# Kernel tuning notes

Measured on AMD Instinct MI355X. Metric: run time of the kernel, lower is better.

The kernel has to match this reference:

```python
import jax, jax.numpy as jnp
import numpy as np

B, H0, W0, D0 = 2, 28, 28, 28
C, NH, SR, WS = 96, 6, 4, 7
N = H0 * W0 * D0
EPS = 1e-5


def _window_partition(x, ws, H, W, D):
    # x: [B, heads, N, c] -> [B*heads*nWindows, ws^3, c]
    Bn, h, Nn, c = x.shape
    x = x.reshape(Bn * h, H // ws, ws, W // ws, ws, D // ws, ws, c)
    x = x.transpose(0, 1, 3, 5, 2, 4, 6, 7)
    return x.reshape(-1, ws * ws * ws, c)


def _window_reverse(w, ws, H, W, D, heads):
    # w: [B*heads*nWindows, ws^3, c] -> [B, N, heads*c]
    c = w.shape[-1]
    nW = (H // ws) * (W // ws) * (D // ws)
    Bh = w.shape[0] // nW
    x = w.reshape(Bh, H // ws, W // ws, D // ws, ws, ws, ws, c)
    x = x.transpose(0, 1, 4, 2, 5, 3, 6, 7).reshape(Bh, H, W, D, c)
    x = x.reshape(Bh // heads, heads, H, W, D, c).transpose(0, 2, 3, 4, 1, 5)
    return x.reshape(Bh // heads, H * W * D, heads * c)


def _ln(x, g, b):
    mu = x.mean(-1, keepdims=True)
    var = ((x - mu) ** 2).mean(-1, keepdims=True)
    return (x - mu) * jax.lax.rsqrt(var + EPS) * g + b


def _forward(x, H, W, D, lepe_lin_w, lepe_lin_b, lepe_conv_w, lepe_conv_b,
             sr_w, sr_b, norm_g, norm_b, q1_w, kv1_w, q2_w, kv2_w, proj_w, proj_b):
    Bn, Nn, Cc = x.shape
    nh2 = NH // 2
    hd = Cc // NH
    scale = hd ** -0.5
    dn = ('NCDHW', 'OIDHW', 'NCDHW')
    # LePE branch: linear -> depthwise 3x3x3 conv over the 3D volume
    t = (x @ lepe_lin_w.T + lepe_lin_b).transpose(0, 2, 1).reshape(Bn, Cc, H, W, D)
    lepe = jax.lax.conv_general_dilated(t, lepe_conv_w, (1, 1, 1), [(1, 1)] * 3,
                                        dimension_numbers=dn, feature_group_count=Cc)
    lepe = (lepe + lepe_conv_b[None, :, None, None, None]).reshape(Bn, Cc, Nn).transpose(0, 2, 1)
    # Branch 1: spatial-reduction global attention on half the heads
    q1 = (x @ q1_w.T).reshape(Bn, Nn, nh2, hd).transpose(0, 2, 1, 3)  # [B,h/2,N,hd]
    x5 = x.transpose(0, 2, 1).reshape(Bn, Cc, H, W, D)
    xs = jax.lax.conv_general_dilated(x5, sr_w, (SR, SR, SR), 'VALID', dimension_numbers=dn)
    xs = (xs + sr_b[None, :, None, None, None]).reshape(Bn, Cc, -1).transpose(0, 2, 1)  # [B,Nsr,C]
    xs = jax.nn.gelu(_ln(xs, norm_g, norm_b), approximate=False)
    kv1 = (xs @ kv1_w.T).reshape(Bn, -1, 2, nh2, hd).transpose(2, 0, 3, 1, 4)
    k1, v1 = kv1[0], kv1[1]
    attn1 = jax.nn.softmax(jnp.einsum('bhnd,bhmd->bhnm', q1, k1) * scale, axis=-1)
    x1 = jnp.einsum('bhnm,bhmd->bhnd', attn1, v1).transpose(0, 2, 1, 3).reshape(Bn, Nn, Cc // 2)
    # Branch 2: 7x7x7 windowed local attention on the other half of the heads
    q2 = (x @ q2_w.T).reshape(Bn, Nn, nh2, hd).transpose(0, 2, 1, 3)
    kv2 = (x @ kv2_w.T).reshape(Bn, Nn, 2, nh2, hd).transpose(2, 0, 3, 1, 4)
    k2, v2 = kv2[0], kv2[1]
    q2w = _window_partition(q2, WS, H, W, D)
    k2w = _window_partition(k2, WS, H, W, D)
    v2w = _window_partition(v2, WS, H, W, D)
    attn2 = jax.nn.softmax(jnp.einsum('wnd,wmd->wnm', q2w, k2w) * scale, axis=-1)
    x2 = _window_reverse(jnp.einsum('wnm,wmd->wnd', attn2, v2w), WS, H, W, D, nh2)
    # Fuse branches, add LePE, project
    return (jnp.concatenate([x1, x2], axis=-1) + lepe) @ proj_w.T + proj_b


def setup_inputs() -> dict:
    key = jax.random.key(0)
    ks = jax.random.split(key, 10)
    lin = lambda k, o, i: jax.random.normal(k, (o, i), jnp.float32) * 0.02
    return {
        'x': jax.random.normal(ks[0], (B, N, C), jnp.float32),
        'H': H0, 'W': W0, 'D': D0,
        'lepe_lin_w': lin(ks[1], C, C),
        'lepe_lin_b': jnp.zeros((C,), jnp.float32),
        'lepe_conv_w': jax.random.normal(ks[2], (C, 1, 3, 3, 3), jnp.float32) * 0.27,
        'lepe_conv_b': jnp.zeros((C,), jnp.float32),
        'sr_w': jax.random.normal(ks[3], (C, C, SR, SR, SR), jnp.float32) * 0.02,
        'sr_b': jnp.zeros((C,), jnp.float32),
        'norm_g': jnp.ones((C,), jnp.float32),
        'norm_b': jnp.zeros((C,), jnp.float32),
        'q1_w': lin(ks[4], C // 2, C),
        'kv1_w': lin(ks[5], C, C),
        'q2_w': lin(ks[6], C // 2, C),
        'kv2_w': lin(ks[7], C, C),
        'proj_w': lin(ks[8], C, C),
        'proj_b': jnp.zeros((C,), jnp.float32),
    }


def reference(x, H, W, D, lepe_lin_w, lepe_lin_b, lepe_conv_w, lepe_conv_b,
              sr_w, sr_b, norm_g, norm_b, q1_w, kv1_w, q2_w, kv2_w, proj_w, proj_b):
    return _forward(x, H, W, D, lepe_lin_w, lepe_lin_b, lepe_conv_w, lepe_conv_b,
                    sr_w, sr_b, norm_g, norm_b, q1_w, kv1_w, q2_w, kv2_w, proj_w, proj_b)
```

## Files before the change

### kernel.cpp

```cpp
#include <hip/hip_runtime.h>

#define BB 2
#define NTOK 21952
#define CC 96
#define WD 784
#define NSR 343
#define NKT 22
#define NPADK 9.f
#define NSITE 686
#define SCALE 0.25f
#define LN_EPS 1e-5f
#define WSA_N (6*16*24*64)
#define WPA_N (18*6*64)
#define PSTR 192
#define PLANE ((size_t)BB * NTOK)

typedef _Float16 half_t;
typedef __attribute__((ext_vector_type(2))) _Float16 h2;
typedef __attribute__((ext_vector_type(4))) _Float16 h4;
typedef __attribute__((ext_vector_type(8))) _Float16 h8;
typedef __attribute__((ext_vector_type(4))) float f32x4;
union HU { h8 v; h2 p[4]; };
union H4U { h4 v; h2 p[2]; };

__device__ __forceinline__ h2 pk2(float a, float b) {
    return __builtin_bit_cast(h2, __builtin_amdgcn_cvt_pkrtz(a, b));
}

__global__ __launch_bounds__(256) void k_wt(
    const float* __restrict__ w, h4* __restrict__ WSA, h4* __restrict__ WPA,
    const float* __restrict__ lepe_w, const float* __restrict__ q1_w,
    const float* __restrict__ q2_w, const float* __restrict__ kv2_w,
    const float* __restrict__ cw, float* __restrict__ cwT)
{
    const int id = blockIdx.x * 256 + threadIdx.x;
    if (id < WSA_N) {
        const int lane = id & 63;
        const int kt = (id >> 6) % 24;
        const int ks = ((id >> 6) / 24) % 16;
        const int ct = (id >> 6) / 384;
        const int co = ct * 16 + (lane & 15);
        const int kb = ks * 384 + kt * 16 + 4 * (lane >> 4);
        const int p = kb / 96, c = kb % 96;
        float f[4];
#pragma unroll
        for (int i = 0; i < 4; i++)
            f[i] = w[(size_t)co * 6144 + (c + i) * 64 + p];
        H4U t; t.p[0] = pk2(f[0], f[1]); t.p[1] = pk2(f[2], f[3]);
        WSA[id] = t.v;
    } else if (id < WSA_N + WPA_N) {
        const int id2 = id - WSA_N;
        const int lane = id2 & 63;
        const int kt = (id2 >> 6) % 6;
        const int ct = (id2 >> 6) / 6;
        const int co = ct * 16 + (lane & 15);
        const int k = kt * 16 + 4 * (lane >> 4);
        const float* wrow;
        if (co < 96)       wrow = lepe_w + co * 96;
        else if (co < 144) wrow = q1_w + (co - 96) * 96;
        else if (co < 192) wrow = q2_w + (co - 144) * 96;
        else               wrow = kv2_w + (co - 192) * 96;
        float4 v = *(const float4*)(wrow + k);
        H4U t; t.p[0] = pk2(v.x, v.y); t.p[1] = pk2(v.z, v.w);
        WPA[id2] = t.v;
    } else if (id < WSA_N + WPA_N + 27 * 96) {
        const int id3 = id - WSA_N - WPA_N;
        const int tap = id3 / 96, c = id3 % 96;
        cwT[tap * 96 + c] = cw[c * 27 + tap];
    }
}

__global__ __launch_bounds__(256) void k_proj(
    const float* __restrict__ x, const h4* __restrict__ WPA,
    const float* __restrict__ lepe_b, float* __restrict__ P,
    float4* __restrict__ tl)
{
    __shared__ h4 BX[4 * 6 * 64];
    const int blk = blockIdx.x;
    const int tid = threadIdx.x;

    for (int s = tid; s < 1536; s += 256) {
        int lane = s & 63;
        int kt = (s >> 6) % 6;
        int tt = (s >> 6) / 6;
        int tok = blk * 64 + tt * 16 + (lane & 15);
        int k0 = kt * 16 + 4 * (lane >> 4);
        float4 v = *(const float4*)(x + (size_t)tok * 96 + k0);
        H4U t; t.p[0] = pk2(v.x, v.y); t.p[1] = pk2(v.z, v.w);
        BX[s] = t.v;
    }
    __syncthreads();

    const int lane = tid & 63;
    const int wid = tid >> 6;

    h4 bx[24];
#pragma unroll
    for (int q = 0; q < 24; q++) bx[q] = BX[q * 64 + lane];

    for (int ct = wid; ct < 18; ct += 4) {
        f32x4 acc[4];
#pragma unroll
        for (int tt = 0; tt < 4; tt++) acc[tt] = (f32x4){0.f, 0.f, 0.f, 0.f};
#pragma unroll
        for (int kt = 0; kt < 6; kt++) {
            h4 wa = WPA[(ct * 6 + kt) * 64 + lane];
#pragma unroll
            for (int tt = 0; tt < 4; tt++)
                acc[tt] = __builtin_amdgcn_mfma_f32_16x16x16f16(
                    wa, bx[tt * 6 + kt], acc[tt], 0, 0, 0);
        }
        if (ct < 6) {
            float4 b4 = *(const float4*)(lepe_b + ct * 16 + 4 * (lane >> 4));
            const size_t cg = ct * 4 + (lane >> 4);
#pragma unroll
            for (int tt = 0; tt < 4; tt++) {
                int tok = blk * 64 + tt * 16 + (lane & 15);
                tl[cg * PLANE + tok] =
                    make_float4(acc[tt][0] + b4.x, acc[tt][1] + b4.y,
                                acc[tt][2] + b4.z, acc[tt][3] + b4.w);
            }
        } else {
#pragma unroll
            for (int tt = 0; tt < 4; tt++) {
                int tok = blk * 64 + tt * 16 + (lane & 15);
                *(float4*)(P + (size_t)tok * PSTR + (ct - 6) * 16
                           + 4 * (lane >> 4)) =
                    make_float4(acc[tt][0], acc[tt][1], acc[tt][2], acc[tt][3]);
            }
        }
    }
}

__global__ __launch_bounds__(384) void k_sr_a(
    const float* __restrict__ x, const h4* __restrict__ WSA,
    float* __restrict__ pa)
{
    __shared__ h4 BX[24 * 64];
    const int mb = blockIdx.x;
    const int ks = blockIdx.y;
    const int tid = threadIdx.x;
    const int lane = tid & 63;
    const int ct = tid >> 6;

    for (int s = tid; s < 24 * 64; s += 384) {
        int l = s & 63;
        int kt = s >> 6;
        int site = mb * 16 + (l & 15);
        if (site > NSITE - 1) site = NSITE - 1;
        int b = site / NSR, sloc = site % NSR;
        int si = sloc / 49, sj = (sloc / 7) % 7, sk = sloc % 7;
        int kg = ks * 384 + kt * 16 + 4 * (l >> 4);
        int p = kg / 96, c = kg % 96;
        int a = p >> 4, q = (p >> 2) & 3, r = p & 3;
        int n = (4 * si + a) * WD + (4 * sj + q) * 28 + (4 * sk + r);
        float4 v = *(const float4*)(x + ((size_t)b * NTOK + n) * 96 + c);
        H4U t; t.p[0] = pk2(v.x, v.y); t.p[1] = pk2(v.z, v.w);
        BX[s] = t.v;
    }
    __syncthreads();

    const int site_g = mb * 16 + (lane & 15);
    const h4* wb = WSA + (size_t)((ct * 16 + ks) * 24) * 64 + lane;

    f32x4 acc0 = (f32x4){0.f, 0.f, 0.f, 0.f};
    f32x4 acc1 = (f32x4){0.f, 0.f, 0.f, 0.f};
#pragma unroll
    for (int kp = 0; kp < 12; kp++) {
        h4 wa0 = wb[(2 * kp) * 64];
        h4 wa1 = wb[(2 * kp + 1) * 64];
        acc0 = __builtin_amdgcn_mfma_f32_16x16x16f16(
            wa0, BX[(2 * kp) * 64 + lane], acc0, 0, 0, 0);
        acc1 = __builtin_amdgcn_mfma_f32_16x16x16f16(
            wa1, BX[(2 * kp + 1) * 64 + lane], acc1, 0, 0, 0);
    }
    if (site_g < NSITE) {
        *(float4*)(pa + ((size_t)site_g * 16 + ks) * 96 + ct * 16
                   + 4 * (lane >> 4)) =
            make_float4(acc0[0] + acc1[0], acc0[1] + acc1[1],
                        acc0[2] + acc1[2], acc0[3] + acc1[3]);
    }
}

__global__ __launch_bounds__(96) void k_sr_b(
    const float* __restrict__ pa, const float* __restrict__ sr_b,
    const float* __restrict__ norm_g, const float* __restrict__ norm_b,
    const float* __restrict__ kv1_w, float* __restrict__ k1,
    float* __restrict__ v1)
{
    __shared__ float xs_s[96];
    __shared__ float gx[96];
    const int s_g = blockIdx.x;
    const int b = s_g / NSR, s = s_g % NSR;
    const int co = threadIdx.x;

    const float* pp = pa + (size_t)s_g * 16 * 96 + co;
    float acc = sr_b[co];
#pragma unroll
    for (int ks = 0; ks < 16; ks++) acc += pp[ks * 96];
    xs_s[co] = acc;
    __syncthreads();

    float m = 0.f, m2 = 0.f;
    for (int c = 0; c < 96; c++) { float v = xs_s[c]; m += v; m2 += v * v; }
    m *= (1.f / 96.f);
    float var = m2 * (1.f / 96.f) - m * m;
    float t = (acc - m) * rsqrtf(var + LN_EPS) * norm_g[co] + norm_b[co];
    gx[co] = 0.5f * t * (1.f + erff(t * 0.70710678118654752f));
    __syncthreads();

    const float4* w4 = (const float4*)(kv1_w + co * 96);
    const float4* g4 = (const float4*)gx;
    float a2 = 0.f;
#pragma unroll
    for (int c = 0; c < 24; c++) {
        float4 w = w4[c]; float4 g = g4[c];
        a2 += g.x * w.x + g.y * w.y + g.z * w.z + g.w * w.w;
    }
    int pair = co / 48, h = (co % 48) / 16, e = co % 16;
    float* dst = pair ? v1 : k1;
    dst[(((size_t)b * 3 + h) * NSR + s) * 16 + e] = a2;
}

__device__ __forceinline__ void attn_mfma_core(
    const h4* __restrict__ KA, const h4* __restrict__ VA, int lane,
    h4 qb, f32x4& o, float& lsum)
{
    o = (f32x4){0.f, 0.f, 0.f, 0.f};
    lsum = 0.f;
    for (int t = 0; t < NKT; t++) {
        h4 ka = KA[t * 64 + lane];
        f32x4 s = __builtin_amdgcn_mfma_f32_16x16x16f16(
            ka, qb, (f32x4){0.f, 0.f, 0.f, 0.f}, 0, 0, 0);
        float p0 = __expf(s[0]), p1 = __expf(s[1]);
        float p2 = __expf(s[2]), p3 = __expf(s[3]);
        lsum += (p0 + p1) + (p2 + p3);
        H4U pb;
        pb.p[0] = pk2(p0, p1);
        pb.p[1] = pk2(p2, p3);
        h4 va = VA[t * 64 + lane];
        o = __builtin_amdgcn_mfma_f32_16x16x16f16(va, pb.v, o, 0, 0, 0);
    }
}

__global__ __launch_bounds__(512) void k_attn(
    const float* __restrict__ P, const float* __restrict__ k1,
    const float* __restrict__ v1, float4* __restrict__ yp)
{
    __shared__ h4 KA[NKT * 64];
    __shared__ h4 VA[NKT * 64];

    if (blockIdx.x < 516) {
        const int bh = blockIdx.x % 6;
        const int qg = blockIdx.x / 6;
        const int b = bh / 3, h = bh % 3;
        const float* ksrc = k1 + (size_t)bh * NSR * 16;
        const float* vsrc = v1 + (size_t)bh * NSR * 16;

        for (int s = threadIdx.x; s < NKT * 64; s += 512) {
            int t = s >> 6, l = s & 63;
            int key = t * 16 + (l & 15);
            int dg = (l >> 4) * 4;
            H4U tmp; tmp.p[0] = pk2(0.f, 0.f); tmp.p[1] = pk2(0.f, 0.f);
            if (key < NSR) {
                float4 v = *(const float4*)(ksrc + (size_t)key * 16 + dg);
                tmp.p[0] = pk2(v.x, v.y); tmp.p[1] = pk2(v.z, v.w);
            }
            KA[s] = tmp.v;
        }
        for (int s = threadIdx.x; s < NKT * 64; s += 512) {
            int t = s >> 6, l = s & 63;
            int dim = l & 15;
            int k0 = t * 16 + (l >> 4) * 4;
            float f[4];
#pragma unroll
            for (int i = 0; i < 4; i++) {
                int key = k0 + i;
                f[i] = (key < NSR) ? vsrc[(size_t)key * 16 + dim] : 0.f;
            }
            H4U tmp; tmp.p[0] = pk2(f[0], f[1]); tmp.p[1] = pk2(f[2], f[3]);
            VA[s] = tmp.v;
        }
        __syncthreads();

        const int lane = threadIdx.x & 63;
        const int wid = threadIdx.x >> 6;

        for (int qi = wid; qi < 16; qi += 8) {
            int qt = qg * 16 + qi;
            if (qt >= 1372) break;
            int tok = qt * 16 + (lane & 15);
            float4 qv = *(const float4*)(P + ((size_t)b * NTOK + tok) * PSTR
                                         + h * 16 + (lane >> 4) * 4);
            H4U qb;
            qb.p[0] = pk2(qv.x * SCALE, qv.y * SCALE);
            qb.p[1] = pk2(qv.z * SCALE, qv.w * SCALE);

            f32x4 o; float lsum;
            attn_mfma_core(KA, VA, lane, qb.v, o, lsum);
            lsum += __shfl_xor(lsum, 16);
            lsum += __shfl_xor(lsum, 32);
            float inv = 1.f / (lsum - NPADK);
            yp[(size_t)(h * 4 + (lane >> 4)) * PLANE + (size_t)b * NTOK + tok] =
                make_float4(o[0] * inv, o[1] * inv, o[2] * inv, o[3] * inv);
        }
        return;
    }

    const int pb = blockIdx.x - 516;
    const int b = pb / 192;
    const int rem = pb % 192;
    const int h = rem / 64, win = rem % 64;
    const int wh = win >> 4, ww = (win >> 2) & 3, wd = win & 3;
    const int h0 = wh * 7, w0 = ww * 7, d0 = wd * 7;
    const size_t bOff = (size_t)b * NTOK;

    for (int s = threadIdx.x; s < NKT * 64; s += 512) {
        int t = s >> 6, l = s & 63;
        int key = t * 16 + (l & 15);
        int dg = (l >> 4) * 4;
        H4U tmp; tmp.p[0] = pk2(0.f, 0.f); tmp.p[1] = pk2(0.f, 0.f);
        if (key < NSR) {
            int a = key / 49, bw = (key / 7) % 7, cw = key % 7;
            int n = (h0 + a) * WD + (w0 + bw) * 28 + (d0 + cw);
            float4 v = *(const float4*)(P + (bOff + n) * PSTR + 96 + h * 16 + dg);
            tmp.p[0] = pk2(v.x, v.y); tmp.p[1] = pk2(v.z, v.w);
        }
        KA[s] = tmp.v;
    }
    for (int s = threadIdx.x; s < NKT * 64; s += 512) {
        int t = s >> 6, l = s & 63;
        int dim = l & 15;
        int k0 = t * 16 + (l >> 4) * 4;
        float f[4];
#pragma unroll
        for (int i = 0; i < 4; i++) {
            int key = k0 + i;
            float val = 0.f;
            if (key < NSR) {
                int a = key / 49, bw = (key / 7) % 7, cw = key % 7;
                int n = (h0 + a) * WD + (w0 + bw) * 28 + (d0 + cw);
                val = P[(bOff + n) * PSTR + 144 + h * 16 + dim];
            }
            f[i] = val;
        }
        H4U tmp; tmp.p[0] = pk2(f[0], f[1]); tmp.p[1] = pk2(f[2], f[3]);
        VA[s] = tmp.v;
    }
    __syncthreads();

    const int lane = threadIdx.x & 63;
    const int wid = threadIdx.x >> 6;

    for (int qt = wid; qt < NKT; qt += 8) {
        int q = qt * 16 + (lane & 15);
        int qc = (q < NSR) ? q : (NSR - 1);
        int ai = qc / 49, bi = (qc / 7) % 7, ci = qc % 7;
        int tok = (h0 + ai) * WD + (w0 + bi) * 28 + (d0 + ci);
        float4 qv = *(const float4*)(P + (bOff + tok) * PSTR
                                     + 48 + h * 16 + (lane >> 4) * 4);
        H4U qb;
        qb.p[0] = pk2(qv.x * SCALE, qv.y * SCALE);
        qb.p[1] = pk2(qv.z * SCALE, qv.w * SCALE);

        f32x4 o; float lsum;
        attn_mfma_core(KA, VA, lane, qb.v, o, lsum);
        lsum += __shfl_xor(lsum, 16);
        lsum += __shfl_xor(lsum, 32);
        float inv = 1.f / (lsum - NPADK);
        if (q < NSR) {
            yp[(size_t)(12 + h * 4 + (lane >> 4)) * PLANE + bOff + tok] =
                make_float4(o[0] * inv, o[1] * inv, o[2] * inv, o[3] * inv);
        }
    }
}

__global__ __launch_bounds__(128) void k_lepe(
    const float4* __restrict__ tl, const float* __restrict__ cwT,
    const float* __restrict__ cb, float4* __restrict__ yp)
{
    const int blk = blockIdx.x;
    const int h = blk % 28;
    const int cg = (blk / 28) % 24;
    const int b = blk / (28 * 24);
    const int t = threadIdx.x;
    if (t >= 112) return;
    const int w = t >> 2;
    const int dq = t & 3;
    const int d0 = dq * 7;
    const int c4 = cg * 4;

    const float4* base = tl + (size_t)cg * PLANE + (size_t)b * NTOK;

    float4 bias = *(const float4*)(cb + c4);
    float4 acc[7];
#pragma unroll
    for (int j = 0; j < 7; j++) acc[j] = bias;

#pragma unroll
    for (int dh = -1; dh <= 1; dh++) {
        const int hh = h + dh;
        const bool hok = (unsigned)hh < 28u;

        float4 pv[3][9];
#pragma unroll
        for (int dwi = 0; dwi < 3; dwi++) {
            const int ww = w + dwi - 1;
            const bool pok = hok & ((unsigned)ww < 28u);
            const float4* pp = base + (pok ? (hh * WD + ww * 28)
                                           : (h * WD + w * 28));
#pragma unroll
            for (int k = 0; k < 9; k++) {
                const int d = d0 - 1 + k;
                const bool dok = (unsigned)d < 28u;
                float4 v = pp[dok ? d : 0];
                if (!dok) v = make_float4(0.f, 0.f, 0.f, 0.f);
                pv[dwi][k] = v;
            }
        }

#pragma unroll
        for (int dwi = 0; dwi < 3; dwi++) {
            const int ww = w + dwi - 1;
            const bool pok = hok & ((unsigned)ww < 28u);
            const float mp = pok ? 1.f : 0.f;
            const int tb = ((dh + 1) * 3 + dwi) * 3;
            float4 wm = *(const float4*)(cwT + (tb + 0) * 96 + c4);
            float4 w0v = *(const float4*)(cwT + (tb + 1) * 96 + c4);
            float4 wp = *(const float4*)(cwT + (tb + 2) * 96 + c4);
            wm.x *= mp; wm.y *= mp; wm.z *= mp; wm.w *= mp;
            w0v.x *= mp; w0v.y *= mp; w0v.z *= mp; w0v.w *= mp;
            wp.x *= mp; wp.y *= mp; wp.z *= mp; wp.w *= mp;
#pragma unroll
            for (int j = 0; j < 7; j++) {
                acc[j].x += pv[dwi][j].x * wm.x + pv[dwi][j + 1].x * w0v.x + pv[dwi][j + 2].x * wp.x;
                acc[j].y += pv[dwi][j].y * wm.y + pv[dwi][j + 1].y * w0v.y + pv[dwi][j + 2].y * wp.y;
                acc[j].z += pv[dwi][j].z * wm.z + pv[dwi][j + 1].z * w0v.z + pv[dwi][j + 2].z * wp.z;
                acc[j].w += pv[dwi][j].w * wm.w + pv[dwi][j + 1].w * w0v.w + pv[dwi][j + 2].w * wp.w;
            }
        }
    }

    float4* yb = yp + (size_t)cg * PLANE + (size_t)b * NTOK
               + h * WD + w * 28 + d0;
#pragma unroll
    for (int j = 0; j < 7; j++) {
        float4 cur = yb[j];
        cur.x += acc[j].x; cur.y += acc[j].y;
        cur.z += acc[j].z; cur.w += acc[j].w;
        yb[j] = cur;
    }
}

__global__ __launch_bounds__(192) void k_out(
    const float4* __restrict__ yp, const float* __restrict__ proj_w,
    const float* __restrict__ proj_b, float* __restrict__ out)
{
    __shared__ h2 xh[48][68];
    __shared__ h2 wh[48][52];

    const int base = blockIdx.x * 64;
    const int j0 = blockIdx.y * 48;

    for (int it = threadIdx.x; it < 1536; it += 192) {
        int t = it & 63, cq = it >> 6;
        float4 v = yp[(size_t)cq * PLANE + base + t];
        xh[cq * 2 + 0][t] = pk2(v.x, v.y);
        xh[cq * 2 + 1][t] = pk2(v.z, v.w);
    }
    for (int it = threadIdx.x; it < 1152; it += 192) {
        int jl = it % 48, cq = it / 48;
        float4 v = *(const float4*)(proj_w + (size_t)(j0 + jl) * 96 + cq * 4);
        wh[cq * 2 + 0][jl] = pk2(v.x, v.y);
        wh[cq * 2 + 1][jl] = pk2(v.z, v.w);
    }
    __syncthreads();

    const int tq = threadIdx.x & 15;
    const int jq = threadIdx.x >> 4;
    float acc[4][4];
#pragma unroll
    for (int i = 0; i < 4; i++)
#pragma unroll
        for (int jj = 0; jj < 4; jj++) acc[i][jj] = 0.f;

    for (int cp = 0; cp < 48; cp++) {
        HU xv, wv;
        xv.v = *(const h8*)(&xh[cp][tq * 4]);
        wv.v = *(const h8*)(&wh[cp][jq * 4]);
#pragma unroll
        for (int i = 0; i < 4; i++)
#pragma unroll
            for (int jj = 0; jj < 4; jj++)
                acc[i][jj] = __builtin_amdgcn_fdot2(xv.p[i], wv.p[jj], acc[i][jj], false);
    }

    float4 bias = *(const float4*)(proj_b + j0 + jq * 4);
#pragma unroll
    for (int i = 0; i < 4; i++) {
        int t = base + tq * 4 + i;
        float4 o = make_float4(acc[i][0] + bias.x, acc[i][1] + bias.y,
                               acc[i][2] + bias.z, acc[i][3] + bias.w);
        *(float4*)(out + (size_t)t * 96 + j0 + jq * 4) = o;
    }
}

extern "C" void kernel_launch(void* const* d_in, const int* in_sizes, int n_in,
                              void* d_out, int out_size, void* d_ws, size_t ws_size,
                              hipStream_t stream) {
    const float* x          = (const float*)d_in[0];
    const float* lepe_lin_w = (const float*)d_in[4];
    const float* lepe_lin_b = (const float*)d_in[5];
    const float* lepe_conv_w= (const float*)d_in[6];
    const float* lepe_conv_b= (const float*)d_in[7];
    const float* sr_w       = (const float*)d_in[8];
    const float* sr_b       = (const float*)d_in[9];
    const float* norm_g     = (const float*)d_in[10];
    const float* norm_b     = (const float*)d_in[11];
    const float* q1_w       = (const float*)d_in[12];
    const float* kv1_w      = (const float*)d_in[13];
    const float* q2_w       = (const float*)d_in[14];
    const float* kv2_w      = (const float*)d_in[15];
    const float* proj_w     = (const float*)d_in[16];
    const float* proj_b     = (const float*)d_in[17];

    float* P   = (float*)d_ws;
    float* tlf = P + (size_t)BB * NTOK * PSTR;
    float* k1  = tlf + (size_t)24 * PLANE * 4;
    float* v1  = k1 + (size_t)BB * 3 * NSR * 16;
    float* ypf = v1 + (size_t)BB * 3 * NSR * 16;
    float* pa  = ypf + (size_t)24 * PLANE * 4;
    float* WSAf= pa + (size_t)NSITE * 16 * 96;
    float* WPAf= WSAf + (size_t)WSA_N * 2;
    float* cwT = WPAf + (size_t)WPA_N * 2;
    h4* WSA = (h4*)WSAf;
    h4* WPA = (h4*)WPAf;
    float4* tl = (float4*)tlf;
    float4* yp = (float4*)ypf;

    k_wt<<<614, 256, 0, stream>>>(sr_w, WSA, WPA, lepe_lin_w, q1_w, q2_w,
                                  kv2_w, lepe_conv_w, cwT);
    k_proj<<<686, 256, 0, stream>>>(x, WPA, lepe_lin_b, P, tl);
    k_sr_a<<<dim3(43, 16), 384, 0, stream>>>(x, WSA, pa);
    k_sr_b<<<NSITE, 96, 0, stream>>>(pa, sr_b, norm_g, norm_b, kv1_w, k1, v1);
    k_attn<<<900, 512, 0, stream>>>(P, k1, v1, yp);
    k_lepe<<<1344, 128, 0, stream>>>(tl, cwT, lepe_conv_b, yp);
    k_out<<<dim3(686, 2), 192, 0, stream>>>(yp, proj_w, proj_b, (float*)d_out);
}
```

Baseline: 198.8 us.

## Merge independent kernels into shared launches and write LePE to separate buffer

Combines the token projection and spatial-reduction GEMM into one launch with block-index dispatch, and merges the depthwise LePE conv into the attention launch as extra blocks. LePE output now goes to a new buffer that the output projection adds in, instead of a read-modify-write on the attention output, removing the ordering dependency between the two. This reduces launch count and lets the independent work run concurrently. In exchange it adds an extra full-size workspace buffer and an extra read in k_out, and the projection blocks leave 128 threads idle.

Result: slower. 257.9 us (+29.7%).

```diff
diff --git a/kernel.cpp b/kernel.cpp
--- a/kernel.cpp
+++ b/kernel.cpp
@@ -70,76 +70,77 @@
     }
 }
 
-__global__ __launch_bounds__(256) void k_proj(
+__global__ __launch_bounds__(384) void k_proj_sra(
     const float* __restrict__ x, const h4* __restrict__ WPA,
     const float* __restrict__ lepe_b, float* __restrict__ P,
-    float4* __restrict__ tl)
-{
-    __shared__ h4 BX[4 * 6 * 64];
-    const int blk = blockIdx.x;
-    const int tid = threadIdx.x;
-
-    for (int s = tid; s < 1536; s += 256) {
-        int lane = s & 63;
-        int kt = (s >> 6) % 6;
-        int tt = (s >> 6) / 6;
-        int tok = blk * 64 + tt * 16 + (lane & 15);
-        int k0 = kt * 16 + 4 * (lane >> 4);
-        float4 v = *(const float4*)(x + (size_t)tok * 96 + k0);
-        H4U t; t.p[0] = pk2(v.x, v.y); t.p[1] = pk2(v.z, v.w);
-        BX[s] = t.v;
-    }
-    __syncthreads();
-
-    const int lane = tid & 63;
-    const int wid = tid >> 6;
-
-    h4 bx[24];
-#pragma unroll
-    for (int q = 0; q < 24; q++) bx[q] = BX[q * 64 + lane];
-
-    for (int ct = wid; ct < 18; ct += 4) {
-        f32x4 acc[4];
-#pragma unroll
-        for (int tt = 0; tt < 4; tt++) acc[tt] = (f32x4){0.f, 0.f, 0.f, 0.f};
-#pragma unroll
-        for (int kt = 0; kt < 6; kt++) {
-            h4 wa = WPA[(ct * 6 + kt) * 64 + lane];
-#pragma unroll
-            for (int tt = 0; tt < 4; tt++)
-                acc[tt] = __builtin_amdgcn_mfma_f32_16x16x16f16(
-                    wa, bx[tt * 6 + kt], acc[tt], 0, 0, 0);
-        }
-        if (ct < 6) {
-            float4 b4 = *(const float4*)(lepe_b + ct * 16 + 4 * (lane >> 4));
-            const size_t cg = ct * 4 + (lane >> 4);
-#pragma unroll
-            for (int tt = 0; tt < 4; tt++) {
-                int tok = blk * 64 + tt * 16 + (lane & 15);
-                tl[cg * PLANE + tok] =
-                    make_float4(acc[tt][0] + b4.x, acc[tt][1] + b4.y,
-                                acc[tt][2] + b4.z, acc[tt][3] + b4.w);
-            }
-        } else {
-#pragma unroll
-            for (int tt = 0; tt < 4; tt++) {
-                int tok = blk * 64 + tt * 16 + (lane & 15);
-                *(float4*)(P + (size_t)tok * PSTR + (ct - 6) * 16
-                           + 4 * (lane >> 4)) =
-                    make_float4(acc[tt][0], acc[tt][1], acc[tt][2], acc[tt][3]);
-            }
-        }
-    }
-}
-
-__global__ __launch_bounds__(384) void k_sr_a(
-    const float* __restrict__ x, const h4* __restrict__ WSA,
+    float4* __restrict__ tl, const h4* __restrict__ WSA,
     float* __restrict__ pa)
 {
-    __shared__ h4 BX[24 * 64];
-    const int mb = blockIdx.x;
-    const int ks = blockIdx.y;
+    __shared__ h4 BX[1536];
     const int tid = threadIdx.x;
+
+    if (blockIdx.x < 686) {
+        const int blk = blockIdx.x;
+        if (tid < 256) {
+            for (int s = tid; s < 1536; s += 256) {
+                int lane = s & 63;
+                int kt = (s >> 6) % 6;
+                int tt = (s >> 6) / 6;
+                int tok = blk * 64 + tt * 16 + (lane & 15);
+                int k0 = kt * 16 + 4 * (lane >> 4);
+                float4 v = *(const float4*)(x + (size_t)tok * 96 + k0);
+                H4U t; t.p[0] = pk2(v.x, v.y); t.p[1] = pk2(v.z, v.w);
+                BX[s] = t.v;
+            }
+        }
+        __syncthreads();
+        if (tid >= 256) return;
+
+        const int lane = tid & 63;
+        const int wid = tid >> 6;
+
+        h4 bx[24];
+#pragma unroll
+        for (int q = 0; q < 24; q++) bx[q] = BX[q * 64 + lane];
+
+        for (int ct = wid; ct < 18; ct += 4) {
+            f32x4 acc[4];
+#pragma unroll
+            for (int tt = 0; tt < 4; tt++) acc[tt] = (f32x4){0.f, 0.f, 0.f, 0.f};
+#pragma unroll
+            for (int kt = 0; kt < 6; kt++) {
+                h4 wa = WPA[(ct * 6 + kt) * 64 + lane];
+#pragma unroll
+                for (int tt = 0; tt < 4; tt++)
+                    acc[tt] = __builtin_amdgcn_mfma_f32_16x16x16f16(
+                        wa, bx[tt * 6 + kt], acc[tt], 0, 0, 0);
+            }
+            if (ct < 6) {
+                float4 b4 = *(const float4*)(lepe_b + ct * 16 + 4 * (lane >> 4));
+                const size_t cg = ct * 4 + (lane >> 4);
+#pragma unroll
+                for (int tt = 0; tt < 4; tt++) {
+                    int tok = blk * 64 + tt * 16 + (lane & 15);
+                    tl[cg * PLANE + tok] =
+                        make_float4(acc[tt][0] + b4.x, acc[tt][1] + b4.y,
+                                    acc[tt][2] + b4.z, acc[tt][3] + b4.w);
+                }
+            } else {
+#pragma unroll
+                for (int tt = 0; tt < 4; tt++) {
+                    int tok = blk * 64 + tt * 16 + (lane & 15);
+                    *(float4*)(P + (size_t)tok * PSTR + (ct - 6) * 16
+                               + 4 * (lane >> 4)) =
+                        make_float4(acc[tt][0], acc[tt][1], acc[tt][2], acc[tt][3]);
+                }
+            }
+        }
+        return;
+    }
+
+    const int idx = blockIdx.x - 686;
+    const int mb = idx % 43;
+    const int ks = idx / 43;
     const int lane = tid & 63;
     const int ct = tid >> 6;
 
@@ -243,9 +244,11 @@
     }
 }
 
-__global__ __launch_bounds__(512) void k_attn(
+__global__ __launch_bounds__(512) void k_attn_lepe(
     const float* __restrict__ P, const float* __restrict__ k1,
-    const float* __restrict__ v1, float4* __restrict__ yp)
+    const float* __restrict__ v1, float4* __restrict__ yp,
+    const float4* __restrict__ tl, const float* __restrict__ cwT,
+    const float* __restrict__ cb, float4* __restrict__ lp)
 {
     __shared__ h4 KA[NKT * 64];
     __shared__ h4 VA[NKT * 64];
@@ -307,154 +310,151 @@
         return;
     }
 
-    const int pb = blockIdx.x - 516;
-    const int b = pb / 192;
-    const int rem = pb % 192;
-    const int h = rem / 64, win = rem % 64;
-    const int wh = win >> 4, ww = (win >> 2) & 3, wd = win & 3;
-    const int h0 = wh * 7, w0 = ww * 7, d0 = wd * 7;
-    const size_t bOff = (size_t)b * NTOK;
-
-    for (int s = threadIdx.x; s < NKT * 64; s += 512) {
-        int t = s >> 6, l = s & 63;
-        int key = t * 16 + (l & 15);
-        int dg = (l >> 4) * 4;
-        H4U tmp; tmp.p[0] = pk2(0.f, 0.f); tmp.p[1] = pk2(0.f, 0.f);
-        if (key < NSR) {
-            int a = key / 49, bw = (key / 7) % 7, cw = key % 7;
-            int n = (h0 + a) * WD + (w0 + bw) * 28 + (d0 + cw);
-            float4 v = *(const float4*)(P + (bOff + n) * PSTR + 96 + h * 16 + dg);
-            tmp.p[0] = pk2(v.x, v.y); tmp.p[1] = pk2(v.z, v.w);
-        }
-        KA[s] = tmp.v;
-    }
-    for (int s = threadIdx.x; s < NKT * 64; s += 512) {
-        int t = s >> 6, l = s & 63;
-        int dim = l & 15;
-        int k0 = t * 16 + (l >> 4) * 4;
-        float f[4];
-#pragma unroll
-        for (int i = 0; i < 4; i++) {
-            int key = k0 + i;
-            float val = 0.f;
+    if (blockIdx.x < 900) {
+        const int pb = blockIdx.x - 516;
+        const int b = pb / 192;
+        const int rem = pb % 192;
+        const int h = rem / 64, win = rem % 64;
+        const int wh = win >> 4, ww = (win >> 2) & 3, wd = win & 3;
+        const int h0 = wh * 7, w0 = ww * 7, d0 = wd * 7;
+        const size_t bOff = (size_t)b * NTOK;
+
+        for (int s = threadIdx.x; s < NKT * 64; s += 512) {
+            int t = s >> 6, l = s & 63;
+            int key = t * 16 + (l & 15);
+            int dg = (l >> 4) * 4;
+            H4U tmp; tmp.p[0] = pk2(0.f, 0.f); tmp.p[1] = pk2(0.f, 0.f);
             if (key < NSR) {
                 int a = key / 49, bw = (key / 7) % 7, cw = key % 7;
                 int n = (h0 + a) * WD + (w0 + bw) * 28 + (d0 + cw);
-                val = P[(bOff + n) * PSTR + 144 + h * 16 + dim];
-            }
-            f[i] = val;
-        }
-        H4U tmp; tmp.p[0] = pk2(f[0], f[1]); tmp.p[1] = pk2(f[2], f[3]);
-        VA[s] = tmp.v;
-    }
-    __syncthreads();
-
-    const int lane = threadIdx.x & 63;
-    const int wid = threadIdx.x >> 6;
-
-    for (int qt = wid; qt < NKT; qt += 8) {
-        int q = qt * 16 + (lane & 15);
-        int qc = (q < NSR) ? q : (NSR - 1);
-        int ai = qc / 49, bi = (qc / 7) % 7, ci = qc % 7;
-        int tok = (h0 + ai) * WD + (w0 + bi) * 28 + (d0 + ci);
-        float4 qv = *(const float4*)(P + (bOff + tok) * PSTR
-                                     + 48 + h * 16 + (lane >> 4) * 4);
-        H4U qb;
-        qb.p[0] = pk2(qv.x * SCALE, qv.y * SCALE);
-        qb.p[1] = pk2(qv.z * SCALE, qv.w * SCALE);
-
-        f32x4 o; float lsum;
-        attn_mfma_core(KA, VA, lane, qb.v, o, lsum);
-        lsum += __shfl_xor(lsum, 16);
-        lsum += __shfl_xor(lsum, 32);
-        float inv = 1.f / (lsum - NPADK);
-        if (q < NSR) {
-            yp[(size_t)(12 + h * 4 + (lane >> 4)) * PLANE + bOff + tok] =
-                make_float4(o[0] * inv, o[1] * inv, o[2] * inv, o[3] * inv);
-        }
-    }
-}
-
-__global__ __launch_bounds__(128) void k_lepe(
-    const float4* __restrict__ tl, const float* __restrict__ cwT,
-    const float* __restrict__ cb, float4* __restrict__ yp)
-{
-    const int blk = blockIdx.x;
-    const int h = blk % 28;
-    const int cg = (blk / 28) % 24;
-    const int b = blk / (28 * 24);
-    const int t = threadIdx.x;
-    if (t >= 112) return;
-    const int w = t >> 2;
-    const int dq = t & 3;
-    const int d0 = dq * 7;
-    const int c4 = cg * 4;
-
-    const float4* base = tl + (size_t)cg * PLANE + (size_t)b * NTOK;
-
-    float4 bias = *(const float4*)(cb + c4);
-    float4 acc[7];
-#pragma unroll
-    for (int j = 0; j < 7; j++) acc[j] = bias;
-
-#pragma unroll
-    for (int dh = -1; dh <= 1; dh++) {
-        const int hh = h + dh;
-        const bool hok = (unsigned)hh < 28u;
-
-        float4 pv[3][9];
-#pragma unroll
-        for (int dwi = 0; dwi < 3; dwi++) {
-            const int ww = w + dwi - 1;
-            const bool pok = hok & ((unsigned)ww < 28u);
-            const float4* pp = base + (pok ? (hh * WD + ww * 28)
-                                           : (h * WD + w * 28));
-#pragma unroll
-            for (int k = 0; k < 9; k++) {
-                const int d = d0 - 1 + k;
-                const bool dok = (unsigned)d < 28u;
-                float4 v = pp[dok ? d : 0];
-                if (!dok) v = make_float4(0.f, 0.f, 0.f, 0.f);
-                pv[dwi][k] = v;
-            }
-        }
-
-#pragma unroll
-        for (int dwi = 0; dwi < 3; dwi++) {
-            const int ww = w + dwi - 1;
-            const bool pok = hok & ((unsigned)ww < 28u);
-            const float mp = pok ? 1.f : 0.f;
-            const int tb = ((dh + 1) * 3 + dwi) * 3;
-            float4 wm = *(const float4*)(cwT + (tb + 0) * 96 + c4);
-            float4 w0v = *(const float4*)(cwT + (tb + 1) * 96 + c4);
-            float4 wp = *(const float4*)(cwT + (tb + 2) * 96 + c4);
-            wm.x *= mp; wm.y *= mp; wm.z *= mp; wm.w *= mp;
-            w0v.x *= mp; w0v.y *= mp; w0v.z *= mp; w0v.w *= mp;
-            wp.x *= mp; wp.y *= mp; wp.z *= mp; wp.w *= mp;
-#pragma unroll
-            for (int j = 0; j < 7; j++) {
-                acc[j].x += pv[dwi][j].x * wm.x + pv[dwi][j + 1].x * w0v.x + pv[dwi][j + 2].x * wp.x;
-                acc[j].y += pv[dwi][j].y * wm.y + pv[dwi][j + 1].y * w0v.y + pv[dwi][j + 2].y * wp.y;
-                acc[j].z += pv[dwi][j].z * wm.z + pv[dwi][j + 1].z * w0v.z + pv[dwi][j + 2].z * wp.z;
-                acc[j].w += pv[dwi][j].w * wm.w + pv[dwi][j + 1].w * w0v.w + pv[dwi][j + 2].w * wp.w;
-            }
-        }
-    }
-
-    float4* yb = yp + (size_t)cg * PLANE + (size_t)b * NTOK
-               + h * WD + w * 28 + d0;
-#pragma unroll
-    for (int j = 0; j < 7; j++) {
-        float4 cur = yb[j];
-        cur.x += acc[j].x; cur.y += acc[j].y;
-        cur.z += acc[j].z; cur.w += acc[j].w;
-        yb[j] = cur;
+                float4 v = *(const float4*)(P + (bOff + n) * PSTR + 96 + h * 16 + dg);
+                tmp.p[0] = pk2(v.x, v.y); tmp.p[1] = pk2(v.z, v.w);
+            }
+            KA[s] = tmp.v;
+        }
+        for (int s = threadIdx.x; s < NKT * 64; s += 512) {
+            int t = s >> 6, l = s & 63;
+            int dim = l & 15;
+            int k0 = t * 16 + (l >> 4) * 4;
+            float f[4];
+#pragma unroll
+            for (int i = 0; i < 4; i++) {
+                int key = k0 + i;
+                float val = 0.f;
+                if (key < NSR) {
+                    int a = key / 49, bw = (key / 7) % 7, cw = key % 7;
+                    int n = (h0 + a) * WD + (w0 + bw) * 28 + (d0 + cw);
+                    val = P[(bOff + n) * PSTR + 144 + h * 16 + dim];
+                }
+                f[i] = val;
+            }
+            H4U tmp; tmp.p[0] = pk2(f[0], f[1]); tmp.p[1] = pk2(f[2], f[3]);
+            VA[s] = tmp.v;
+        }
+        __syncthreads();
+
+        const int lane = threadIdx.x & 63;
+        const int wid = threadIdx.x >> 6;
+
+        for (int qt = wid; qt < NKT; qt += 8) {
+            int q = qt * 16 + (lane & 15);
+            int qc = (q < NSR) ? q : (NSR - 1);
+            int ai = qc / 49, bi = (qc / 7) % 7, ci = qc % 7;
+            int tok = (h0 + ai) * WD + (w0 + bi) * 28 + (d0 + ci);
+            float4 qv = *(const float4*)(P + (bOff + tok) * PSTR
+                                         + 48 + h * 16 + (lane >> 4) * 4);
+            H4U qb;
+            qb.p[0] = pk2(qv.x * SCALE, qv.y * SCALE);
+            qb.p[1] = pk2(qv.z * SCALE, qv.w * SCALE);
+
+            f32x4 o; float lsum;
+            attn_mfma_core(KA, VA, lane, qb.v, o, lsum);
+            lsum += __shfl_xor(lsum, 16);
+            lsum += __shfl_xor(lsum, 32);
+            float inv = 1.f / (lsum - NPADK);
+            if (q < NSR) {
+                yp[(size_t)(12 + h * 4 + (lane >> 4)) * PLANE + bOff + tok] =
+                    make_float4(o[0] * inv, o[1] * inv, o[2] * inv, o[3] * inv);
+            }
+        }
+        return;
+    }
+
+    {
+        const int sub = threadIdx.x >> 7;
+        const int t = threadIdx.x & 127;
+        const int lblk = (blockIdx.x - 900) * 4 + sub;
+        const int h = lblk % 28;
+        const int cg = (lblk / 28) % 24;
+        const int b = lblk / (28 * 24);
+        if (t >= 112) return;
+        const int w = t >> 2;
+        const int dq = t & 3;
+        const int d0 = dq * 7;
+        const int c4 = cg * 4;
+
+        const float4* base = tl + (size_t)cg * PLANE + (size_t)b * NTOK;
+
+        float4 bias = *(const float4*)(cb + c4);
+        float4 acc[7];
+#pragma unroll
+        for (int j = 0; j < 7; j++) acc[j] = bias;
+
+#pragma unroll
+        for (int dh = -1; dh <= 1; dh++) {
+            const int hh = h + dh;
+            const bool hok = (unsigned)hh < 28u;
+
+            float4 pv[3][9];
+#pragma unroll
+            for (int dwi = 0; dwi < 3; dwi++) {
+                const int ww = w + dwi - 1;
+                const bool pok = hok & ((unsigned)ww < 28u);
+                const float4* pp = base + (pok ? (hh * WD + ww * 28)
+                                               : (h * WD + w * 28));
+#pragma unroll
+                for (int k = 0; k < 9; k++) {
+                    const int d = d0 - 1 + k;
+                    const bool dok = (unsigned)d < 28u;
+                    float4 v = pp[dok ? d : 0];
+                    if (!dok) v = make_float4(0.f, 0.f, 0.f, 0.f);
+                    pv[dwi][k] = v;
+                }
+            }
+
+#pragma unroll
+            for (int dwi = 0; dwi < 3; dwi++) {
+                const int ww = w + dwi - 1;
+                const bool pok = hok & ((unsigned)ww < 28u);
+                const float mp = pok ? 1.f : 0.f;
+                const int tb = ((dh + 1) * 3 + dwi) * 3;
+                float4 wm = *(const float4*)(cwT + (tb + 0) * 96 + c4);
+                float4 w0v = *(const float4*)(cwT + (tb + 1) * 96 + c4);
+                float4 wp = *(const float4*)(cwT + (tb + 2) * 96 + c4);
+                wm.x *= mp; wm.y *= mp; wm.z *= mp; wm.w *= mp;
+                w0v.x *= mp; w0v.y *= mp; w0v.z *= mp; w0v.w *= mp;
+                wp.x *= mp; wp.y *= mp; wp.z *= mp; wp.w *= mp;
+#pragma unroll
+                for (int j = 0; j < 7; j++) {
+                    acc[j].x += pv[dwi][j].x * wm.x + pv[dwi][j + 1].x * w0v.x + pv[dwi][j + 2].x * wp.x;
+                    acc[j].y += pv[dwi][j].y * wm.y + pv[dwi][j + 1].y * w0v.y + pv[dwi][j + 2].y * wp.y;
+                    acc[j].z += pv[dwi][j].z * wm.z + pv[dwi][j + 1].z * w0v.z + pv[dwi][j + 2].z * wp.z;
+                    acc[j].w += pv[dwi][j].w * wm.w + pv[dwi][j + 1].w * w0v.w + pv[dwi][j + 2].w * wp.w;
+                }
+            }
+        }
+
+        float4* yb = lp + (size_t)cg * PLANE + (size_t)b * NTOK
+                   + h * WD + w * 28 + d0;
+#pragma unroll
+        for (int j = 0; j < 7; j++) yb[j] = acc[j];
     }
 }
 
 __global__ __launch_bounds__(192) void k_out(
-    const float4* __restrict__ yp, const float* __restrict__ proj_w,
-    const float* __restrict__ proj_b, float* __restrict__ out)
+    const float4* __restrict__ yp, const float4* __restrict__ lp,
+    const float* __restrict__ proj_w, const float* __restrict__ proj_b,
+    float* __restrict__ out)
 {
     __shared__ h2 xh[48][68];
     __shared__ h2 wh[48][52];
@@ -465,6 +465,8 @@
     for (int it = threadIdx.x; it < 1536; it += 192) {
         int t = it & 63, cq = it >> 6;
         float4 v = yp[(size_t)cq * PLANE + base + t];
+        float4 l = lp[(size_t)cq * PLANE + base + t];
+        v.x += l.x; v.y += l.y; v.z += l.z; v.w += l.w;
         xh[cq * 2 + 0][t] = pk2(v.x, v.y);
         xh[cq * 2 + 1][t] = pk2(v.z, v.w);
     }
@@ -529,7 +531,8 @@
     float* k1  = tlf + (size_t)24 * PLANE * 4;
     float* v1  = k1 + (size_t)BB * 3 * NSR * 16;
     float* ypf = v1 + (size_t)BB * 3 * NSR * 16;
-    float* pa  = ypf + (size_t)24 * PLANE * 4;
+    float* lpf = ypf + (size_t)24 * PLANE * 4;
+    float* pa  = lpf + (size_t)24 * PLANE * 4;
     float* WSAf= pa + (size_t)NSITE * 16 * 96;
     float* WPAf= WSAf + (size_t)WSA_N * 2;
     float* cwT = WPAf + (size_t)WPA_N * 2;
@@ -537,13 +540,14 @@
     h4* WPA = (h4*)WPAf;
     float4* tl = (float4*)tlf;
     float4* yp = (float4*)ypf;
+    float4* lp = (float4*)lpf;
 
     k_wt<<<614, 256, 0, stream>>>(sr_w, WSA, WPA, lepe_lin_w, q1_w, q2_w,
                                   kv2_w, lepe_conv_w, cwT);
-    k_proj<<<686, 256, 0, stream>>>(x, WPA, lepe_lin_b, P, tl);
-    k_sr_a<<<dim3(43, 16), 384, 0, stream>>>(x, WSA, pa);
+    k_proj_sra<<<1374, 384, 0, stream>>>(x, WPA, lepe_lin_b, P, tl, WSA, pa);
     k_sr_b<<<NSITE, 96, 0, stream>>>(pa, sr_b, norm_g, norm_b, kv1_w, k1, v1);
-    k_attn<<<900, 512, 0, stream>>>(P, k1, v1, yp);
-    k_lepe<<<1344, 128, 0, stream>>>(tl, cwT, lepe_conv_b, yp);
-    k_out<<<dim3(686, 2), 192, 0, stream>>>(yp, proj_w, proj_b, (float*)d_out);
-}
+    k_attn_lepe<<<1236, 512, 0, stream>>>(P, k1, v1, yp, tl, cwT,
+                                          lepe_conv_b, lp);
+    k_out<<<dim3(686, 2), 192, 0, stream>>>(yp, lp, proj_w, proj_b,
+                                            (float*)d_out);
+}
```
